# Kernel tuning notes

Measured on AMD Instinct MI355X. Metric: run time of the kernel, lower is better.

Reference implementation:

```python
import jax, jax.numpy as jnp
import numpy as np
from jax import lax

LOOKBACK = 336
N_FEATURES = 164
HORIZON = 96
D_MODEL = 64
D_STATE = 16
D_CONV = 4
EXPAND = 2
D_INNER = EXPAND * D_MODEL  # 128
DT_RANK = (D_MODEL + 15) // 16  # 4
MLP_HIDDEN = 64
BATCH = 512


def setup_inputs() -> dict:
    key = jax.random.key(0)
    ks = jax.random.split(key, 20)
    f32 = jnp.float32
    inp = {}
    inp["x_raw"] = jax.random.normal(ks[0], (BATCH, LOOKBACK), f32)
    inp["x_features"] = jax.random.normal(ks[1], (BATCH, N_FEATURES), f32)
    # embed Linear(1, d_model)
    inp["embed_W"] = jax.random.normal(ks[2], (1, D_MODEL), f32) * 0.5
    inp["embed_b"] = jnp.zeros((D_MODEL,), f32)
    # Mamba params (mamba-ssm layout, stored as [in, out] for matmul)
    inp["in_W"] = jax.random.normal(ks[3], (D_MODEL, 2 * D_INNER), f32) * (1.0 / np.sqrt(D_MODEL))
    inp["conv_W"] = jax.random.normal(ks[4], (D_INNER, D_CONV), f32) * 0.3
    inp["conv_b"] = jnp.zeros((D_INNER,), f32)
    inp["xproj_W"] = jax.random.normal(ks[5], (D_INNER, DT_RANK + 2 * D_STATE), f32) * (1.0 / np.sqrt(D_INNER))
    inp["dt_W"] = jax.random.normal(ks[6], (DT_RANK, D_INNER), f32) * (1.0 / np.sqrt(DT_RANK))
    inp["dt_b"] = jax.random.uniform(ks[7], (D_INNER,), f32, -4.0, -2.0)  # softplus -> small dt
    # A_log init = log(arange(1..d_state)) broadcast over d_inner, as in mamba-ssm
    inp["A_log"] = jnp.log(jnp.broadcast_to(jnp.arange(1, D_STATE + 1, dtype=f32), (D_INNER, D_STATE)))
    inp["D"] = jnp.ones((D_INNER,), f32)
    inp["out_W"] = jax.random.normal(ks[8], (D_INNER, D_MODEL), f32) * (1.0 / np.sqrt(D_INNER))
    # MLP stream
    inp["mlp_W1"] = jax.random.normal(ks[9], (N_FEATURES, MLP_HIDDEN), f32) * (1.0 / np.sqrt(N_FEATURES))
    inp["mlp_b1"] = jnp.zeros((MLP_HIDDEN,), f32)
    inp["mlp_W2"] = jax.random.normal(ks[10], (MLP_HIDDEN, MLP_HIDDEN // 2), f32) * (1.0 / np.sqrt(MLP_HIDDEN))
    inp["mlp_b2"] = jnp.zeros((MLP_HIDDEN // 2,), f32)
    # prediction head
    fin = D_MODEL + MLP_HIDDEN // 2
    inp["head_W"] = jax.random.normal(ks[11], (fin, HORIZON), f32) * (1.0 / np.sqrt(fin))
    inp["head_b"] = jnp.zeros((HORIZON,), f32)
    return inp


def silu(x):
    return x * jax.nn.sigmoid(x)


def mamba_block(u, in_W, conv_W, conv_b, xproj_W, dt_W, dt_b, A_log, D, out_W):
    # u: [B, L, d_model]
    B_, L, _ = u.shape
    xz = u @ in_W                      # [B, L, 2*D_INNER]
    x, z = jnp.split(xz, 2, axis=-1)   # each [B, L, D_INNER]
    # causal depthwise conv1d (pad left d_conv-1), then SiLU
    xc = x.transpose(0, 2, 1)          # [B, D_INNER, L]
    kern = conv_W[:, None, :]          # [D_INNER, 1, K] (OIH)
    xc = lax.conv_general_dilated(xc, kern, window_strides=(1,),
                                  padding=[(D_CONV - 1, 0)],
                                  dimension_numbers=("NCH", "OIH", "NCH"),
                                  feature_group_count=D_INNER)
    xc = silu(xc + conv_b[None, :, None])
    x = xc.transpose(0, 2, 1)          # [B, L, D_INNER]
    # input-dependent SSM params
    x_dbl = x @ xproj_W                # [B, L, DT_RANK + 2*D_STATE]
    dt = x_dbl[..., :DT_RANK]
    Bm = x_dbl[..., DT_RANK:DT_RANK + D_STATE]          # [B, L, N]
    Cm = x_dbl[..., DT_RANK + D_STATE:]                 # [B, L, N]
    delta = jax.nn.softplus(dt @ dt_W + dt_b)           # [B, L, D_INNER]
    A = -jnp.exp(A_log)                                 # [D_INNER, N]

    # selective scan over time
    def step(h, inps):
        d_t, B_t, C_t, x_t = inps  # [B,Di], [B,N], [B,N], [B,Di]
        dA = jnp.exp(d_t[:, :, None] * A[None])              # [B, Di, N]
        dBx = (d_t * x_t)[:, :, None] * B_t[:, None, :]      # [B, Di, N]
        h = dA * h + dBx
        y_t = jnp.einsum("bdn,bn->bd", h, C_t)
        return h, y_t

    h0 = jnp.zeros((B_, D_INNER, D_STATE), u.dtype)
    seq = (delta.transpose(1, 0, 2), Bm.transpose(1, 0, 2),
           Cm.transpose(1, 0, 2), x.transpose(1, 0, 2))
    _, ys = lax.scan(step, h0, seq)        # ys: [L, B, D_INNER]
    y = ys.transpose(1, 0, 2) + x * D[None, None, :]
    y = y * silu(z)
    return y @ out_W                        # [B, L, d_model]


def reference(x_raw, x_features, embed_W, embed_b, in_W, conv_W, conv_b,
              xproj_W, dt_W, dt_b, A_log, D, out_W,
              mlp_W1, mlp_b1, mlp_W2, mlp_b2, head_W, head_b):
    # embed raw series: [B, L] -> [B, L, 1] -> [B, L, d_model]
    h = x_raw[..., None] @ embed_W + embed_b
    h = mamba_block(h, in_W, conv_W, conv_b, xproj_W, dt_W, dt_b, A_log, D, out_W)
    h_mamba_out = h[:, -1, :]                       # [B, d_model]
    h_mlp = jax.nn.relu(x_features @ mlp_W1 + mlp_b1) @ mlp_W2 + mlp_b2
    h_final = jnp.concatenate([h_mamba_out, h_mlp], axis=1)
    return h_final @ head_W + head_b                # [B, horizon]
```

## Files before the change

### kernel.cpp

```cpp
#include <hip/hip_runtime.h>
#include <math.h>

#define LOOKBACK 336
#define NFEAT    164
#define HORIZON  96
#define DMODEL   64
#define DSTATE   16
#define DINNER   128
#define MLPH     64
#define BATCH    512
#define XCP      132
#define NGL      2
#define GSEG     84
#define CHK      12
#define NCH      7
#define HSTR     20
#define WSB      4736

typedef float v2f __attribute__((ext_vector_type(2)));

__device__ __forceinline__ float fast_rcp(float x) { return __builtin_amdgcn_rcpf(x); }
__device__ __forceinline__ float silu_f(float x) {
    return x * fast_rcp(1.f + __expf(-x));
}

__global__ __launch_bounds__(256, 2) void mamba_scan2(
    const float* __restrict__ x_raw,   const float* __restrict__ x_features,
    const float* __restrict__ embed_W, const float* __restrict__ embed_b,
    const float* __restrict__ in_W,
    const float* __restrict__ conv_W,  const float* __restrict__ conv_b,
    const float* __restrict__ xproj_W, const float* __restrict__ dt_W,
    const float* __restrict__ dt_b,    const float* __restrict__ A_log,
    const float* __restrict__ mlp_W1,  const float* __restrict__ mlp_b1,
    float* __restrict__ ws)
{
    __shared__ __align__(16) float xrl[172];
    __shared__ __align__(16) float xprojT[20*XCP];
    __shared__ __align__(16) float xcbuf[2][NGL][CHK*XCP];
    __shared__ __align__(16) float Bsh[NGL][CHK][DSTATE];
    __shared__ __align__(16) float dtraw[NGL][CHK][4];
    __shared__ __align__(16) float xcl_lds[DINNER];

    const int tid   = threadIdx.x;
    const int batch = blockIdx.x >> 1;
    const int half  = blockIdx.x & 1;
    const int gl    = tid >> 7;
    const int ch    = tid & 127;

    for (int i = tid; i < 171; i += 256) {
        int t = half*168 + i - 3;
        xrl[i] = (t >= 0) ? x_raw[batch*LOOKBACK + t] : 0.f;
    }
    for (int idx = tid; idx < 20*DINNER; idx += 256) {
        int jj = idx >> 7, d = idx & 127;
        xprojT[jj*XCP + d] = xproj_W[d*36 + jj];
    }

    float w1 = 0.f, w0 = 0.f;
    for (int dm = 0; dm < DMODEL; ++dm) {
        float w = in_W[dm*(2*DINNER) + ch];
        w1 = fmaf(embed_W[dm], w, w1);
        w0 = fmaf(embed_b[dm], w, w0);
    }
    const float4 cw = *(const float4*)&conv_W[ch*4];
    const float  cb = conv_b[ch];
    const float dtw0 = dt_W[ch],       dtw1 = dt_W[128 + ch],
                dtw2 = dt_W[256 + ch], dtw3 = dt_W[384 + ch];
    const float dtb_r = dt_b[ch];
    bool structured = true;
    #pragma unroll
    for (int i = 0; i < 16; ++i) {
        float a = __expf(A_log[ch*DSTATE + i]);
        float ex = (float)(i + 1);
        structured = structured && (fabsf(a - ex) < 1e-3f * ex);
    }
    const bool sfast = __all(structured);

    const int a2jp = tid / 12;
    const int a2tt = tid - a2jp*12;
    const int cch = tid & 127;
    __syncthreads();

    {
        float* xw = &xcbuf[0][gl][0];
        const float* xr = &xrl[gl*GSEG];
        if (half == 0 && gl == 0) {
            for (int tt = 0; tt < CHK; ++tt) {
                float acc = cb;
                if (tt >= 3) acc = fmaf(fmaf(xr[tt],   w1, w0), cw.x, acc);
                if (tt >= 2) acc = fmaf(fmaf(xr[tt+1], w1, w0), cw.y, acc);
                if (tt >= 1) acc = fmaf(fmaf(xr[tt+2], w1, w0), cw.z, acc);
                acc = fmaf(fmaf(xr[tt+3], w1, w0), cw.w, acc);
                xw[tt*XCP + ch] = silu_f(acc);
            }
        } else {
            float e0 = fmaf(xr[0], w1, w0);
            float e1 = fmaf(xr[1], w1, w0);
            float e2 = fmaf(xr[2], w1, w0);
            #pragma unroll
            for (int tt = 0; tt < CHK; ++tt) {
                float e3 = fmaf(xr[tt+3], w1, w0);
                float acc = cb + e0*cw.x + e1*cw.y + e2*cw.z + e3*cw.w;
                xw[tt*XCP + ch] = silu_f(acc);
                e0 = e1; e1 = e2; e2 = e3;
            }
        }
    }
    __syncthreads();

    v2f h01={0,0},h23={0,0},h45={0,0},h67={0,0},
        h89={0,0},hAB={0,0},hCD={0,0},hEF={0,0};
    float dacc = 0.f;

    for (int c = 0; c < NCH; ++c) {
        const int buf = c & 1;

        if (tid < 120) {
            const int j0 = a2jp*2;
            const float* p0  = &xprojT[j0*XCP];
            const float* p1  = &xprojT[(j0+1)*XCP];
            const float* xra = &xcbuf[buf][0][a2tt*XCP];
            const float* xrb = &xcbuf[buf][1][a2tt*XCP];
            v2f a0a={0,0}, a1a={0,0}, a0b={0,0}, a1b={0,0};
            #pragma unroll 4
            for (int d = 0; d < DINNER; d += 4) {
                float4 q0 = *(const float4*)(p0 + d);
                float4 q1 = *(const float4*)(p1 + d);
                float4 xa = *(const float4*)(xra + d);
                float4 xb = *(const float4*)(xrb + d);
                v2f q0l={q0.x,q0.y}, q0h={q0.z,q0.w};
                v2f q1l={q1.x,q1.y}, q1h={q1.z,q1.w};
                v2f xal={xa.x,xa.y}, xah={xa.z,xa.w};
                v2f xbl={xb.x,xb.y}, xbh={xb.z,xb.w};
                a0a = __builtin_elementwise_fma(xal, q0l, a0a);
                a0a = __builtin_elementwise_fma(xah, q0h, a0a);
                a1a = __builtin_elementwise_fma(xal, q1l, a1a);
                a1a = __builtin_elementwise_fma(xah, q1h, a1a);
                a0b = __builtin_elementwise_fma(xbl, q0l, a0b);
                a0b = __builtin_elementwise_fma(xbh, q0h, a0b);
                a1b = __builtin_elementwise_fma(xbl, q1l, a1b);
                a1b = __builtin_elementwise_fma(xbh, q1h, a1b);
            }
            float r0a=a0a.x+a0a.y, r1a=a1a.x+a1a.y;
            float r0b=a0b.x+a0b.y, r1b=a1b.x+a1b.y;
            if (j0 < 4) {
                *(float2*)&dtraw[0][a2tt][j0] = make_float2(r0a, r1a);
                *(float2*)&dtraw[1][a2tt][j0] = make_float2(r0b, r1b);
            } else {
                *(float2*)&Bsh[0][a2tt][j0-4] = make_float2(r0a, r1a);
                *(float2*)&Bsh[1][a2tt][j0-4] = make_float2(r0b, r1b);
            }
        } else if (tid >= 128 && c + 1 < NCH) {
            #pragma unroll
            for (int q = 0; q < 2; ++q) {
                float* xw = &xcbuf[buf^1][q][0];
                const float* xr = &xrl[q*GSEG + (c+1)*CHK];
                float e0 = fmaf(xr[0], w1, w0);
                float e1 = fmaf(xr[1], w1, w0);
                float e2 = fmaf(xr[2], w1, w0);
                float v = 0.f;
                #pragma unroll
                for (int tt = 0; tt < CHK; ++tt) {
                    float e3 = fmaf(xr[tt+3], w1, w0);
                    float acc = cb + e0*cw.x + e1*cw.y + e2*cw.z + e3*cw.w;
                    v = silu_f(acc);
                    xw[tt*XCP + cch] = v;
                    e0 = e1; e1 = e2; e2 = e3;
                }
                if (half == 1 && q == 1 && c + 1 == NCH-1) {
                    ws[(size_t)batch*WSB + 4352 + cch] = v;
                    xcl_lds[cch] = v;
                }
            }
        }
        __syncthreads();

        const float* xs = &xcbuf[buf][gl][0];
        if (__builtin_expect(sfast, 1)) {
            #pragma unroll
            for (int tt = 0; tt < CHK; ++tt) {
                float4 dr = *(const float4*)&dtraw[gl][tt][0];
                float dv = fmaf(dr.x, dtw0, fmaf(dr.y, dtw1,
                           fmaf(dr.z, dtw2, fmaf(dr.w, dtw3, dtb_r))));
                float e  = __expf(dv);
                float p  = 1.f + e;
                float r  = fast_rcp(p);
                float dl = (dv > 80.f) ? dv : __logf(p);
                dacc += dl;
                float ux = dl * xs[tt*XCP + ch];
                float4 B0 = *(const float4*)&Bsh[gl][tt][0];
                float4 B1 = *(const float4*)&Bsh[gl][tt][4];
                float4 B2 = *(const float4*)&Bsh[gl][tt][8];
                float4 B3 = *(const float4*)&Bsh[gl][tt][12];
                float r2 = r*r, r4 = r2*r2, r8 = r4*r4;
                v2f r2v = {r2, r2}, r4v = {r4, r4}, r8v = {r8, r8};
                v2f p01 = {r, r2};
                v2f p23 = p01*r2v;
                v2f p45 = p01*r4v, p67 = p23*r4v;
                v2f p89 = p01*r8v, pAB = p23*r8v, pCD = p45*r8v, pEF = p67*r8v;
                v2f uxv = {ux, ux};
                h01 = __builtin_elementwise_fma(p01, h01, uxv*(v2f){B0.x,B0.y});
                h23 = __builtin_elementwise_fma(p23, h23, uxv*(v2f){B0.z,B0.w});
                h45 = __builtin_elementwise_fma(p45, h45, uxv*(v2f){B1.x,B1.y});
                h67 = __builtin_elementwise_fma(p67, h67, uxv*(v2f){B1.z,B1.w});
                h89 = __builtin_elementwise_fma(p89, h89, uxv*(v2f){B2.x,B2.y});
                hAB = __builtin_elementwise_fma(pAB, hAB, uxv*(v2f){B2.z,B2.w});
                hCD = __builtin_elementwise_fma(pCD, hCD, uxv*(v2f){B3.x,B3.y});
                hEF = __builtin_elementwise_fma(pEF, hEF, uxv*(v2f){B3.z,B3.w});
            }
        } else {
            const float* Arow = A_log + ch*DSTATE;
            for (int tt = 0; tt < CHK; ++tt) {
                float4 dr = *(const float4*)&dtraw[gl][tt][0];
                float dv = fmaf(dr.x, dtw0, fmaf(dr.y, dtw1,
                           fmaf(dr.z, dtw2, fmaf(dr.w, dtw3, dtb_r))));
                float e  = __expf(dv);
                float dl = (dv > 15.f) ? dv : __logf(1.f + e);
                dacc += dl;
                float ux = dl * xs[tt*XCP + ch];
                const float* Brow = &Bsh[gl][tt][0];
                float hv[16] = {h01.x,h01.y,h23.x,h23.y,h45.x,h45.y,h67.x,h67.y,
                                h89.x,h89.y,hAB.x,hAB.y,hCD.x,hCD.y,hEF.x,hEF.y};
                for (int i = 0; i < 16; ++i)
                    hv[i] = fmaf(__expf(-__expf(Arow[i])*dl), hv[i], ux*Brow[i]);
                h01=(v2f){hv[0],hv[1]};   h23=(v2f){hv[2],hv[3]};
                h45=(v2f){hv[4],hv[5]};   h67=(v2f){hv[6],hv[7]};
                h89=(v2f){hv[8],hv[9]};   hAB=(v2f){hv[10],hv[11]};
                hCD=(v2f){hv[12],hv[13]}; hEF=(v2f){hv[14],hv[15]};
            }
        }
        __syncthreads();
    }

    float* hpart = &xcbuf[0][0][0];
    float* dsum  = &Bsh[0][0][0];
    float* Cpart = &Bsh[0][0][0] + 128;
    if (gl == 0) {
        float4* hp = (float4*)&hpart[ch*HSTR];
        hp[0] = make_float4(h01.x,h01.y,h23.x,h23.y);
        hp[1] = make_float4(h45.x,h45.y,h67.x,h67.y);
        hp[2] = make_float4(h89.x,h89.y,hAB.x,hAB.y);
        hp[3] = make_float4(hCD.x,hCD.y,hEF.x,hEF.y);
        dsum[ch] = dacc;
    }
    __syncthreads();
    if (gl == 1) {
        const float4* hp = (const float4*)&hpart[ch*HSTR];
        float4 a = hp[0], bq = hp[1], cq = hp[2], dq = hp[3];
        float h0[16] = {a.x,a.y,a.z,a.w,bq.x,bq.y,bq.z,bq.w,
                        cq.x,cq.y,cq.z,cq.w,dq.x,dq.y,dq.z,dq.w};
        float h1[16] = {h01.x,h01.y,h23.x,h23.y,h45.x,h45.y,h67.x,h67.y,
                        h89.x,h89.y,hAB.x,hAB.y,hCD.x,hCD.y,hEF.x,hEF.y};
        float P[16];
        if (structured) {
            float r = __expf(-dacc);
            float pw = 1.f;
            #pragma unroll
            for (int i = 0; i < 16; ++i) { pw *= r; P[i] = fmaf(pw, h0[i], h1[i]); }
        } else {
            #pragma unroll
            for (int i = 0; i < 16; ++i)
                P[i] = fmaf(__expf(-__expf(A_log[ch*DSTATE+i])*dacc), h0[i], h1[i]);
        }
        float* wsb = ws + (size_t)batch*WSB + half*2176;
        float4* pw4 = (float4*)(wsb + ch*16);
        pw4[0] = make_float4(P[0],P[1],P[2],P[3]);
        pw4[1] = make_float4(P[4],P[5],P[6],P[7]);
        pw4[2] = make_float4(P[8],P[9],P[10],P[11]);
        pw4[3] = make_float4(P[12],P[13],P[14],P[15]);
        wsb[2048 + ch] = dsum[ch] + dacc;
    }

    if (half == 0) {
        if (tid < 128) {
            float a1 = 0.f, a0 = 0.f;
            for (int dm = 0; dm < DMODEL; ++dm) {
                float w = in_W[dm*(2*DINNER) + DINNER + tid];
                a1 = fmaf(embed_W[dm], w, a1);
                a0 = fmaf(embed_b[dm], w, a0);
            }
            float x335 = x_raw[batch*LOOKBACK + 335];
            ws[(size_t)batch*WSB + 4480 + tid] = silu_f(fmaf(x335, a1, a0));
        } else {
            const int lane = tid - 128;
            const int j = lane >> 1, k = lane & 1;
            const float* xf = x_features + batch*NFEAT;
            float acc = 0.f;
            const int f0 = k*82, f1 = (k ? NFEAT : 82);
            for (int f = f0; f < f1; ++f)
                acc = fmaf(xf[f], mlp_W1[f*MLPH + j], acc);
            acc += __shfl_xor(acc, 1);
            if (k == 0)
                ws[(size_t)batch*WSB + 4608 + j] = fmaxf(acc + mlp_b1[j], 0.f);
        }
    } else {
        if (tid < 128) {
            const int q = tid >> 4, n = tid & 15;
            float acc = 0.f;
            for (int d = q*16; d < q*16 + 16; ++d)
                acc = fmaf(xcl_lds[d], xproj_W[d*36 + 20 + n], acc);
            Cpart[q*16 + n] = acc;
        }
        __syncthreads();
        if (tid < 16) {
            float s = 0.f;
            #pragma unroll
            for (int q = 0; q < 8; ++q) s += Cpart[q*16 + tid];
            ws[(size_t)batch*WSB + 4672 + tid] = s;
        }
    }
}

__global__ __launch_bounds__(256, 2) void mamba_epi(
    const float* __restrict__ A_log,   const float* __restrict__ Dvec,
    const float* __restrict__ out_W,
    const float* __restrict__ mlp_W2,  const float* __restrict__ mlp_b2,
    const float* __restrict__ head_W,  const float* __restrict__ head_b,
    const float* __restrict__ ws,      float* __restrict__ out)
{
    __shared__ float yv[DINNER], hfin[96];

    const int tid = threadIdx.x;
    const int b   = blockIdx.x;
    const float* wsb = ws + (size_t)b*WSB;

    if (tid < 128) {
        const int ch = tid;
        bool structured = true;
        #pragma unroll
        for (int i = 0; i < 16; ++i) {
            float a = __expf(A_log[ch*DSTATE + i]);
            float ex = (float)(i + 1);
            structured = structured && (fabsf(a - ex) < 1e-3f * ex);
        }
        const float4* p01 = (const float4*)(wsb + ch*16);
        const float4* p23 = (const float4*)(wsb + 2176 + ch*16);
        float D23 = wsb[2176 + 2048 + ch];
        float4 a0 = p01[0], a1 = p01[1], a2 = p01[2], a3 = p01[3];
        float4 b0 = p23[0], b1 = p23[1], b2 = p23[2], b3 = p23[3];
        float P0[16] = {a0.x,a0.y,a0.z,a0.w,a1.x,a1.y,a1.z,a1.w,
                        a2.x,a2.y,a2.z,a2.w,a3.x,a3.y,a3.z,a3.w};
        float P1[16] = {b0.x,b0.y,b0.z,b0.w,b1.x,b1.y,b1.z,b1.w,
                        b2.x,b2.y,b2.z,b2.w,b3.x,b3.y,b3.z,b3.w};
        float H[16];
        if (structured) {
            float r = __expf(-D23);
            float pw = 1.f;
            #pragma unroll
            for (int i = 0; i < 16; ++i) { pw *= r; H[i] = fmaf(pw, P0[i], P1[i]); }
        } else {
            #pragma unroll
            for (int i = 0; i < 16; ++i)
                H[i] = fmaf(__expf(-__expf(A_log[ch*DSTATE+i])*D23), P0[i], P1[i]);
        }
        const float* Cl = wsb + 4672;
        float acc = 0.f;
        #pragma unroll
        for (int i = 0; i < 16; ++i) acc = fmaf(H[i], Cl[i], acc);
        float y = acc + wsb[4352 + ch]*Dvec[ch];
        yv[ch] = y * wsb[4480 + ch];
    } else {
        const int lane = tid - 128;
        const int j = lane >> 2, k = lane & 3;
        const float* mlph = wsb + 4608;
        float acc = 0.f;
        for (int kk = k*16; kk < k*16 + 16; ++kk)
            acc = fmaf(mlph[kk], mlp_W2[kk*32 + j], acc);
        acc += __shfl_xor(acc, 1);
        acc += __shfl_xor(acc, 2);
        if (k == 0) hfin[64 + j] = acc + mlp_b2[j];
    }
    __syncthreads();

    {
        const int o = tid >> 2, k = tid & 3;
        float acc = 0.f;
        for (int d = k*32; d < k*32 + 32; ++d)
            acc = fmaf(yv[d], out_W[d*DMODEL + o], acc);
        acc += __shfl_xor(acc, 1);
        acc += __shfl_xor(acc, 2);
        if (k == 0) hfin[o] = acc;
    }
    __syncthreads();

    if (tid < 192) {
        const int o = tid >> 1, k = tid & 1;
        float acc = 0.f;
        for (int i = k*48; i < k*48 + 48; ++i)
            acc = fmaf(hfin[i], head_W[i*HORIZON + o], acc);
        acc += __shfl_xor(acc, 1);
        if (k == 0) out[b*HORIZON + o] = acc + head_b[o];
    }
}

extern "C" void kernel_launch(void* const* d_in, const int* in_sizes, int n_in,
                              void* d_out, int out_size, void* d_ws, size_t ws_size,
                              hipStream_t stream) {
    (void)in_sizes; (void)n_in; (void)out_size; (void)ws_size;
    float* ws = (float*)d_ws;
    mamba_scan2<<<BATCH*2, 256, 0, stream>>>(
        (const float*)d_in[0],  (const float*)d_in[1],
        (const float*)d_in[2],  (const float*)d_in[3],  (const float*)d_in[4],
        (const float*)d_in[5],  (const float*)d_in[6],  (const float*)d_in[7],
        (const float*)d_in[8],  (const float*)d_in[9],  (const float*)d_in[10],
        (const float*)d_in[13], (const float*)d_in[14],
        ws);
    mamba_epi<<<BATCH, 256, 0, stream>>>(
        (const float*)d_in[10], (const float*)d_in[11], (const float*)d_in[12],
        (const float*)d_in[15], (const float*)d_in[16], (const float*)d_in[17],
        (const float*)d_in[18], ws, (float*)d_out);
}
```

Before: 173.0 us.

## Move z-gate, C projection and MLP layer-1 from scan kernel into epilogue

```diff
diff --git a/kernel.cpp b/kernel.cpp
--- a/kernel.cpp
+++ b/kernel.cpp
@@ -15,7 +15,7 @@
 #define CHK      12
 #define NCH      7
 #define HSTR     20
-#define WSB      4736
+#define WSB      4480
 
 typedef float v2f __attribute__((ext_vector_type(2)));
 
@@ -25,13 +25,12 @@
 }
 
 __global__ __launch_bounds__(256, 2) void mamba_scan2(
-    const float* __restrict__ x_raw,   const float* __restrict__ x_features,
+    const float* __restrict__ x_raw,
     const float* __restrict__ embed_W, const float* __restrict__ embed_b,
     const float* __restrict__ in_W,
     const float* __restrict__ conv_W,  const float* __restrict__ conv_b,
     const float* __restrict__ xproj_W, const float* __restrict__ dt_W,
     const float* __restrict__ dt_b,    const float* __restrict__ A_log,
-    const float* __restrict__ mlp_W1,  const float* __restrict__ mlp_b1,
     float* __restrict__ ws)
 {
     __shared__ __align__(16) float xrl[172];
@@ -39,7 +38,6 @@
     __shared__ __align__(16) float xcbuf[2][NGL][CHK*XCP];
     __shared__ __align__(16) float Bsh[NGL][CHK][DSTATE];
     __shared__ __align__(16) float dtraw[NGL][CHK][4];
-    __shared__ __align__(16) float xcl_lds[DINNER];
 
     const int tid   = threadIdx.x;
     const int batch = blockIdx.x >> 1;
@@ -167,10 +165,8 @@
                     xw[tt*XCP + cch] = v;
                     e0 = e1; e1 = e2; e2 = e3;
                 }
-                if (half == 1 && q == 1 && c + 1 == NCH-1) {
+                if (half == 1 && q == 1 && c + 1 == NCH-1)
                     ws[(size_t)batch*WSB + 4352 + cch] = v;
-                    xcl_lds[cch] = v;
-                }
             }
         }
         __syncthreads();
@@ -234,7 +230,6 @@
 
     float* hpart = &xcbuf[0][0][0];
     float* dsum  = &Bsh[0][0][0];
-    float* Cpart = &Bsh[0][0][0] + 128;
     if (gl == 0) {
         float4* hp = (float4*)&hpart[ch*HSTR];
         hp[0] = make_float4(h01.x,h01.y,h23.x,h23.y);
@@ -270,59 +265,27 @@
         pw4[3] = make_float4(P[12],P[13],P[14],P[15]);
         wsb[2048 + ch] = dsum[ch] + dacc;
     }
-
-    if (half == 0) {
-        if (tid < 128) {
-            float a1 = 0.f, a0 = 0.f;
-            for (int dm = 0; dm < DMODEL; ++dm) {
-                float w = in_W[dm*(2*DINNER) + DINNER + tid];
-                a1 = fmaf(embed_W[dm], w, a1);
-                a0 = fmaf(embed_b[dm], w, a0);
-            }
-            float x335 = x_raw[batch*LOOKBACK + 335];
-            ws[(size_t)batch*WSB + 4480 + tid] = silu_f(fmaf(x335, a1, a0));
-        } else {
-            const int lane = tid - 128;
-            const int j = lane >> 1, k = lane & 1;
-            const float* xf = x_features + batch*NFEAT;
-            float acc = 0.f;
-            const int f0 = k*82, f1 = (k ? NFEAT : 82);
-            for (int f = f0; f < f1; ++f)
-                acc = fmaf(xf[f], mlp_W1[f*MLPH + j], acc);
-            acc += __shfl_xor(acc, 1);
-            if (k == 0)
-                ws[(size_t)batch*WSB + 4608 + j] = fmaxf(acc + mlp_b1[j], 0.f);
-        }
-    } else {
-        if (tid < 128) {
-            const int q = tid >> 4, n = tid & 15;
-            float acc = 0.f;
-            for (int d = q*16; d < q*16 + 16; ++d)
-                acc = fmaf(xcl_lds[d], xproj_W[d*36 + 20 + n], acc);
-            Cpart[q*16 + n] = acc;
-        }
-        __syncthreads();
-        if (tid < 16) {
-            float s = 0.f;
-            #pragma unroll
-            for (int q = 0; q < 8; ++q) s += Cpart[q*16 + tid];
-            ws[(size_t)batch*WSB + 4672 + tid] = s;
-        }
-    }
 }
 
 __global__ __launch_bounds__(256, 2) void mamba_epi(
+    const float* __restrict__ x_raw,   const float* __restrict__ x_features,
+    const float* __restrict__ embed_W, const float* __restrict__ embed_b,
+    const float* __restrict__ in_W,    const float* __restrict__ xproj_W,
     const float* __restrict__ A_log,   const float* __restrict__ Dvec,
     const float* __restrict__ out_W,
+    const float* __restrict__ mlp_W1,  const float* __restrict__ mlp_b1,
     const float* __restrict__ mlp_W2,  const float* __restrict__ mlp_b2,
     const float* __restrict__ head_W,  const float* __restrict__ head_b,
     const float* __restrict__ ws,      float* __restrict__ out)
 {
-    __shared__ float yv[DINNER], hfin[96];
+    __shared__ float Cpart[8][16], Cl[DSTATE];
+    __shared__ float yv[DINNER], hfin[96], mlph[MLPH];
 
     const int tid = threadIdx.x;
     const int b   = blockIdx.x;
     const float* wsb = ws + (size_t)b*WSB;
+
+    float H[16], zs = 0.f;
 
     if (tid < 128) {
         const int ch = tid;
@@ -336,39 +299,86 @@
         const float4* p01 = (const float4*)(wsb + ch*16);
         const float4* p23 = (const float4*)(wsb + 2176 + ch*16);
         float D23 = wsb[2176 + 2048 + ch];
-        float4 a0 = p01[0], a1 = p01[1], a2 = p01[2], a3 = p01[3];
-        float4 b0 = p23[0], b1 = p23[1], b2 = p23[2], b3 = p23[3];
-        float P0[16] = {a0.x,a0.y,a0.z,a0.w,a1.x,a1.y,a1.z,a1.w,
-                        a2.x,a2.y,a2.z,a2.w,a3.x,a3.y,a3.z,a3.w};
-        float P1[16] = {b0.x,b0.y,b0.z,b0.w,b1.x,b1.y,b1.z,b1.w,
-                        b2.x,b2.y,b2.z,b2.w,b3.x,b3.y,b3.z,b3.w};
-        float H[16];
         if (structured) {
             float r = __expf(-D23);
             float pw = 1.f;
             #pragma unroll
-            for (int i = 0; i < 16; ++i) { pw *= r; H[i] = fmaf(pw, P0[i], P1[i]); }
+            for (int w = 0; w < 4; ++w) {
+                float4 a0 = p01[w], b0 = p23[w];
+                float q0[4] = {a0.x,a0.y,a0.z,a0.w};
+                float q1[4] = {b0.x,b0.y,b0.z,b0.w};
+                #pragma unroll
+                for (int j = 0; j < 4; ++j) {
+                    pw *= r;
+                    H[w*4 + j] = fmaf(pw, q0[j], q1[j]);
+                }
+            }
         } else {
             #pragma unroll
-            for (int i = 0; i < 16; ++i)
-                H[i] = fmaf(__expf(-__expf(A_log[ch*DSTATE+i])*D23), P0[i], P1[i]);
-        }
-        const float* Cl = wsb + 4672;
+            for (int w = 0; w < 4; ++w) {
+                float4 a0 = p01[w], b0 = p23[w];
+                float q0[4] = {a0.x,a0.y,a0.z,a0.w};
+                float q1[4] = {b0.x,b0.y,b0.z,b0.w};
+                #pragma unroll
+                for (int j = 0; j < 4; ++j) {
+                    float aa = __expf(-__expf(A_log[ch*DSTATE + w*4 + j])*D23);
+                    H[w*4 + j] = fmaf(aa, q0[j], q1[j]);
+                }
+            }
+        }
+        float a1 = 0.f, a0 = 0.f;
+        for (int dm = 0; dm < DMODEL; ++dm) {
+            float w = in_W[dm*(2*DINNER) + DINNER + ch];
+            a1 = fmaf(embed_W[dm], w, a1);
+            a0 = fmaf(embed_b[dm], w, a0);
+        }
+        zs = silu_f(fmaf(x_raw[b*LOOKBACK + 335], a1, a0));
+    } else {
+        const int lane = tid - 128;
+        {
+            const int q = lane >> 4, n = lane & 15;
+            const float* xcw = wsb + 4352;
+            float acc = 0.f;
+            for (int d = q*16; d < q*16 + 16; ++d)
+                acc = fmaf(xcw[d], xproj_W[d*36 + 20 + n], acc);
+            Cpart[q][n] = acc;
+        }
+        {
+            const int j = lane >> 1, k = lane & 1;
+            const float* xf = x_features + b*NFEAT;
+            float acc = 0.f;
+            const int f0 = k*82, f1 = (k ? NFEAT : 82);
+            for (int f = f0; f < f1; ++f)
+                acc = fmaf(xf[f], mlp_W1[f*MLPH + j], acc);
+            acc += __shfl_xor(acc, 1);
+            if (k == 0) mlph[j] = fmaxf(acc + mlp_b1[j], 0.f);
+        }
+    }
+    __syncthreads();
+
+    if (tid >= 128 && tid < 144) {
+        const int n = tid - 128;
+        float s = 0.f;
+        #pragma unroll
+        for (int q = 0; q < 8; ++q) s += Cpart[q][n];
+        Cl[n] = s;
+    } else if (tid >= 144 && tid < 208) {
+        const int lane = tid - 144;
+        const int j = lane >> 1, k = lane & 1;
+        float acc = 0.f;
+        for (int kk = k*32; kk < k*32 + 32; ++kk)
+            acc = fmaf(mlph[kk], mlp_W2[kk*32 + j], acc);
+        acc += __shfl_xor(acc, 1);
+        if (k == 0) hfin[64 + j] = acc + mlp_b2[j];
+    }
+    __syncthreads();
+
+    if (tid < 128) {
         float acc = 0.f;
         #pragma unroll
         for (int i = 0; i < 16; ++i) acc = fmaf(H[i], Cl[i], acc);
-        float y = acc + wsb[4352 + ch]*Dvec[ch];
-        yv[ch] = y * wsb[4480 + ch];
-    } else {
-        const int lane = tid - 128;
-        const int j = lane >> 2, k = lane & 3;
-        const float* mlph = wsb + 4608;
-        float acc = 0.f;
-        for (int kk = k*16; kk < k*16 + 16; ++kk)
-            acc = fmaf(mlph[kk], mlp_W2[kk*32 + j], acc);
-        acc += __shfl_xor(acc, 1);
-        acc += __shfl_xor(acc, 2);
-        if (k == 0) hfin[64 + j] = acc + mlp_b2[j];
+        float y = acc + wsb[4352 + tid]*Dvec[tid];
+        yv[tid] = y * zs;
     }
     __syncthreads();
 
@@ -399,14 +409,16 @@
     (void)in_sizes; (void)n_in; (void)out_size; (void)ws_size;
     float* ws = (float*)d_ws;
     mamba_scan2<<<BATCH*2, 256, 0, stream>>>(
-        (const float*)d_in[0],  (const float*)d_in[1],
+        (const float*)d_in[0],
         (const float*)d_in[2],  (const float*)d_in[3],  (const float*)d_in[4],
         (const float*)d_in[5],  (const float*)d_in[6],  (const float*)d_in[7],
         (const float*)d_in[8],  (const float*)d_in[9],  (const float*)d_in[10],
-        (const float*)d_in[13], (const float*)d_in[14],
         ws);
     mamba_epi<<<BATCH, 256, 0, stream>>>(
+        (const float*)d_in[0],  (const float*)d_in[1],  (const float*)d_in[2],
+        (const float*)d_in[3],  (const float*)d_in[4],  (const float*)d_in[7],
         (const float*)d_in[10], (const float*)d_in[11], (const float*)d_in[12],
-        (const float*)d_in[15], (const float*)d_in[16], (const float*)d_in[17],
-        (const float*)d_in[18], ws, (float*)d_out);
+        (const float*)d_in[13], (const float*)d_in[14], (const float*)d_in[15],
+        (const float*)d_in[16], (const float*)d_in[17], (const float*)d_in[18],
+        ws, (float*)d_out);
 }
```

Measured after the change: 189.3 us. 1.09x slower.
